# Performance work log

Measured on AMD Instinct MI355X. Metric: run time of the kernel, lower is better.

The kernel has to match this reference:

```python
import jax, jax.numpy as jnp
import numpy as np
from jax.scipy.linalg import expm

D_LOGIC = 128
D_MEM = 16
SO_DIM = D_MEM * (D_MEM - 1) // 2  # 120


def _linear_init(key, fan_in, shape):
    bound = 1.0 / np.sqrt(fan_in)
    return jax.random.uniform(key, shape, jnp.float32, -bound, bound)


def setup_inputs() -> dict:
    key = jax.random.key(0)
    ks = jax.random.split(key, 14)
    B, S = 4, 128
    return {
        "x_logic": jax.random.normal(ks[0], (B, S, D_LOGIC), jnp.float32),
        "x_memory": jax.random.normal(ks[1], (B, S, D_MEM), jnp.float32),
        # W_Q / W_K
        "Wq": _linear_init(ks[2], D_LOGIC, (D_LOGIC, D_LOGIC)),
        "bq": _linear_init(ks[3], D_LOGIC, (D_LOGIC,)),
        "Wk": _linear_init(ks[4], D_LOGIC, (D_LOGIC, D_LOGIC)),
        "bk": _linear_init(ks[5], D_LOGIC, (D_LOGIC,)),
        # gamma_net: Linear(d_logic, 2*d_logic) -> Tanh -> Linear(2*d_logic, so_dim)
        "W1": _linear_init(ks[6], D_LOGIC, (2 * D_LOGIC, D_LOGIC)),
        "b1": _linear_init(ks[7], D_LOGIC, (2 * D_LOGIC,)),
        "W2": _linear_init(ks[8], 2 * D_LOGIC, (SO_DIM, 2 * D_LOGIC)),
        "b2": _linear_init(ks[9], 2 * D_LOGIC, (SO_DIM,)),
        # out_proj: Linear(d_memory, d_memory)
        "Wo": _linear_init(ks[10], D_MEM, (D_MEM, D_MEM)),
        "bo": _linear_init(ks[11], D_MEM, (D_MEM,)),
    }


def reference(x_logic, x_memory, Wq, bq, Wk, bk, W1, b1, W2, b2, Wo, bo):
    B, S, d_logic = x_logic.shape
    dm = x_memory.shape[-1]

    # attention over logic stream
    Q = x_logic @ Wq.T + bq
    K = x_logic @ Wk.T + bk
    attn = jax.nn.softmax(
        jnp.einsum("bjd,bid->bji", Q, K) / jnp.sqrt(jnp.float32(d_logic)), axis=-1
    )  # [B, S(j), S(i)]

    # per-pair Lie-algebra params: delta[b,j,i] = x_logic[b,j] - x_logic[b,i]
    delta = x_logic[:, :, None, :] - x_logic[:, None, :, :]  # [B,S,S,d_logic]
    h = jnp.tanh(delta @ W1.T + b1)
    lie = h @ W2.T + b2  # [B,S,S,so_dim]

    # scatter into skew-symmetric matrices [B,S,S,dm,dm]
    r, c = np.triu_indices(dm, k=1)
    skew = jnp.zeros((B, S, S, dm, dm), x_logic.dtype)
    skew = skew.at[..., r, c].set(lie)
    skew = skew.at[..., c, r].set(-lie)

    # Lie-group exponential -> orthogonal transport matrices
    T_all = expm(skew)  # [B,S,S,dm,dm]

    # transported[b,j,i,:] = T[b,j,i] @ x_memory[b,i]
    transported = jnp.einsum("bjide,bie->bjid", T_all, x_memory)

    # attention-weighted aggregation over i
    settled = jnp.einsum("bji,bjid->bjd", attn, transported)  # [B,S,dm]

    out = settled @ Wo.T + bo
    return out, T_all
```

## Files before the change

### kernel.cpp

```cpp
#include <hip/hip_runtime.h>
#include <hip/hip_fp16.h>

#define S_LEN 128
#define DLOG  128
#define DMEM  16
#define SO    120
#define HDIM  256

typedef _Float16 v8h __attribute__((ext_vector_type(8)));
typedef __fp16 v2hf __attribute__((ext_vector_type(2)));
typedef float v4f __attribute__((ext_vector_type(4)));

union PkU { v2hf h; unsigned u; };
union V8U { v8h v; int u[4]; };

__device__ __forceinline__ v8h splat8(float x) {
  _Float16 h = (_Float16)x;
  v8h v = {h, h, h, h, h, h, h, h};
  return v;
}

__global__ __launch_bounds__(512) void qku_kernel(
    const float* __restrict__ xl, const float* __restrict__ Wq,
    const float* __restrict__ bq, const float* __restrict__ Wk,
    const float* __restrict__ bk, const float* __restrict__ W1,
    float* __restrict__ Q, float* __restrict__ K, float* __restrict__ u) {
  int bj = blockIdx.x, t = threadIdx.x;
  __shared__ float xs[128];
  if (t < 128) xs[t] = xl[bj * 128 + t];
  __syncthreads();
  const float* wr;
  float acc;
  int o;
  if (t < 128) {
    o = t; wr = Wq + o * 128; acc = bq[o];
  } else if (t < 256) {
    o = t - 128; wr = Wk + o * 128; acc = bk[o];
  } else {
    o = t - 256; wr = W1 + o * 128; acc = 0.f;
  }
  #pragma unroll 4
  for (int d = 0; d < 128; ++d) acc = fmaf(xs[d], wr[d], acc);
  if (t < 128) Q[bj * 128 + o] = acc;
  else if (t < 256) K[bj * 128 + o] = acc;
  else u[bj * 256 + o] = acc;
}

__global__ __launch_bounds__(128) void attn_kernel(
    const float* __restrict__ Q, const float* __restrict__ K,
    float* __restrict__ attn) {
  int bj = blockIdx.x, b = bj >> 7, i = threadIdx.x;
  __shared__ float qs[128];
  __shared__ float red[128];
  qs[i] = Q[bj * 128 + i];
  __syncthreads();
  const float* kr = K + (b * 128 + i) * 128;
  float s = 0.f;
  #pragma unroll 4
  for (int d = 0; d < 128; ++d) s = fmaf(qs[d], kr[d], s);
  s *= 0.08838834764831845f;
  red[i] = s;
  __syncthreads();
  for (int off = 64; off; off >>= 1) {
    if (i < off) red[i] = fmaxf(red[i], red[i + off]);
    __syncthreads();
  }
  float m = red[0];
  __syncthreads();
  float e = expf(s - m);
  red[i] = e;
  __syncthreads();
  for (int off = 64; off; off >>= 1) {
    if (i < off) red[i] += red[i + off];
    __syncthreads();
  }
  attn[(size_t)bj * 128 + i] = e / red[0];
}

__global__ __launch_bounds__(256) void w2prep_kernel(
    const float* __restrict__ W2g, _Float16* __restrict__ w2h) {
  int idx = (blockIdx.x * 256 + threadIdx.x) * 4;
  float4 v = *(const float4*)(W2g + idx);
  PkU u0, u1;
  u0.h = __builtin_amdgcn_cvt_pkrtz(v.x, v.y);
  u1.h = __builtin_amdgcn_cvt_pkrtz(v.z, v.w);
  uint2 pk = {u0.u, u1.u};
  *(uint2*)(w2h + idx) = pk;
}

__global__ __launch_bounds__(256) void h_from_u_kernel(
    const float* __restrict__ u, const float* __restrict__ b1,
    _Float16* __restrict__ hG) {
  int tid = blockIdx.x * 256 + threadIdx.x;
  #pragma unroll
  for (int g = 0; g < 4; ++g) {
    int unit = tid + g * 524288;
    int p = unit >> 5;
    int o0 = (unit & 31) * 8;
    int bj = p >> 7;
    int b = bj >> 7;
    int i = p & 127;
    const float* uj = u + bj * 256 + o0;
    const float* ui = u + (size_t)(b * 128 + i) * 256 + o0;
    const float* bb = b1 + o0;
    float4 j0 = *(const float4*)uj, j1 = *(const float4*)(uj + 4);
    float4 i0 = *(const float4*)ui, i1 = *(const float4*)(ui + 4);
    float4 c0 = *(const float4*)bb, c1 = *(const float4*)(bb + 4);
    float xv[8] = {j0.x - i0.x + c0.x, j0.y - i0.y + c0.y,
                   j0.z - i0.z + c0.z, j0.w - i0.w + c0.w,
                   j1.x - i1.x + c1.x, j1.y - i1.y + c1.y,
                   j1.z - i1.z + c1.z, j1.w - i1.w + c1.w};
    float rv[8];
    #pragma unroll
    for (int k = 0; k < 8; ++k) {
      float x = xv[k];
      float ax = fabsf(x);
      float e = __expf(-2.f * ax);
      float r = __fdividef(1.f - e, 1.f + e);
      rv[k] = copysignf(r, x);
    }
    V8U out;
    #pragma unroll
    for (int k = 0; k < 4; ++k) {
      PkU pu;
      pu.h = __builtin_amdgcn_cvt_pkrtz(rv[2 * k], rv[2 * k + 1]);
      out.u[k] = (int)pu.u;
    }
    *(v8h*)(hG + (size_t)p * 512 + o0) = out.v;
  }
}

__global__ __launch_bounds__(512) void lie_kernel(
    const _Float16* __restrict__ w2h, const float* __restrict__ b2g,
    float* __restrict__ Tg) {
  __shared__ _Float16 w2t[128 * 136];
  int t = threadIdx.x, lane = t & 63;
  int wu = __builtin_amdgcn_readfirstlane(t >> 6);
  int pbase = blockIdx.x * 128 + wu * 16;
  int nn = lane & 15, q = lane >> 4;
  const _Float16* hf = (const _Float16*)Tg;

  for (int idx = t; idx < 1088; idx += 512) w2t[16320 + idx] = (_Float16)0.f;

  v4f acc[8];
  #pragma unroll
  for (int tt = 0; tt < 8; ++tt) acc[tt] = (v4f){0.f, 0.f, 0.f, 0.f};

  const _Float16* hrow = hf + (size_t)(pbase + nn) * 512;
  for (int khalf = 0; khalf < 2; ++khalf) {
    __syncthreads();
    for (int idx = t; idx < 1920; idx += 512) {
      int row = idx >> 4, cu = (idx & 15) * 8;
      *(v8h*)(w2t + row * 136 + cu) =
          *(const v8h*)(w2h + row * 256 + khalf * 128 + cu);
    }
    __syncthreads();
    #pragma unroll
    for (int ks = 0; ks < 4; ++ks) {
      v8h ah = *(const v8h*)(hrow + khalf * 128 + ks * 32 + 8 * q);
      #pragma unroll
      for (int tt = 0; tt < 8; ++tt) {
        const v8h bf = *(const v8h*)(w2t + (16 * tt + nn) * 136 + ks * 32 + 8 * q);
        acc[tt] = __builtin_amdgcn_mfma_f32_16x16x32_f16(ah, bf, acc[tt], 0, 0, 0);
      }
    }
  }

  _Float16* hw = (_Float16*)Tg;
  #pragma unroll
  for (int tt = 0; tt < 8; ++tt) {
    int n16 = 16 * tt + nn;
    if (n16 < 120) {
      float bb = b2g[n16];
      #pragma unroll
      for (int reg = 0; reg < 4; ++reg) {
        size_t p = (size_t)(pbase + 4 * q + reg);
        hw[p * 512 + 256 + n16] = (_Float16)(acc[tt][reg] + bb);
      }
    }
  }
}

__device__ __forceinline__ void split8(const float* x, v8h& hi, v8h& lo) {
  union U { v8h v; v2hf p[4]; } H, L;
  #pragma unroll
  for (int i = 0; i < 4; ++i) {
    float a = x[2 * i], b = x[2 * i + 1];
    v2hf h = __builtin_amdgcn_cvt_pkrtz(a, b);
    float ra = (float)h[0], rb = (float)h[1];
    v2hf l = __builtin_amdgcn_cvt_pkrtz(a - ra, b - rb);
    H.p[i] = h;
    L.p[i] = l;
  }
  hi = H.v;
  lo = L.v;
}

__device__ __forceinline__ int lie_idx(int rr, int cc) {
  return 15 * rr - ((rr * (rr - 1)) >> 1) + cc - rr - 1;
}

__global__ __launch_bounds__(256) void expm_kernel(
    float* __restrict__ Tg, const float* __restrict__ attn,
    const float* __restrict__ xm, float* __restrict__ part) {
  __shared__ char lds[12288] __attribute__((aligned(16)));
  __shared__ float sred[4][16];
  int t = threadIdx.x, lane = t & 63;
  int wu = __builtin_amdgcn_readfirstlane(t >> 6);
  int pbase = blockIdx.x * 8 + wu * 2;
  int nn = lane & 15, q = lane >> 4, b8 = (q & 1) * 8;
  char* wb = lds + wu * 3072;
  _Float16* lieS = (_Float16*)wb;
  float* ErB = (float*)(wb + 512);
  const _Float16* hf = (const _Float16*)Tg;

  int idxA = ((2 * (q & 1)) * 16 + nn) * 4;
  int idxB = idxA + 64;

  float scv[2];
  int sv[2];
  #pragma unroll
  for (int j = 0; j < 2; ++j) {
    size_t p = (size_t)(pbase + j);
    _Float16 a0 = (lane < 120) ? hf[p * 512 + 256 + lane] : (_Float16)0.f;
    _Float16 a1 = (lane < 56) ? hf[p * 512 + 320 + lane] : (_Float16)0.f;
    lieS[j * 128 + lane] = a0;
    lieS[j * 128 + 64 + lane] = a1;
    float f0 = (float)a0, f1 = (float)a1;
    float s2 = f0 * f0 + f1 * f1;
    #pragma unroll
    for (int off = 1; off < 64; off <<= 1) s2 += __shfl_xor(s2, off, 64);
    float bound = sqrtf(s2);
    int s = 0;
    while (bound > 1.0f && s < 12) { bound *= 0.5f; s++; }
    sv[j] = __builtin_amdgcn_readfirstlane(s);
    scv[j] = ldexpf(1.0f, -s);
  }
  asm volatile("s_waitcnt lgkmcnt(0)" ::: "memory");

  V8U Apk[2], BfA[2];
  v4f Af[2];
  #pragma unroll
  for (int j = 0; j < 2; ++j) {
    const _Float16* lp = lieS + j * 128;
    float sc = scv[j];
    float av[8];
    #pragma unroll
    for (int jj = 0; jj < 8; ++jj) {
      int c = b8 + jj;
      int rr = min(nn, c), c2 = max(nn, c);
      float lv = (c == nn) ? 0.f : (float)lp[lie_idx(rr, c2)];
      av[jj] = (c == nn) ? 0.f : ((c > nn) ? lv : -lv) * sc;
    }
    #pragma unroll
    for (int i = 0; i < 4; ++i) {
      PkU u;
      u.h = __builtin_amdgcn_cvt_pkrtz(av[2 * i], av[2 * i + 1]);
      Apk[j].u[i] = (int)u.u;
      BfA[j].u[i] = Apk[j].u[i] ^ 0x80008000;
    }
    #pragma unroll
    for (int reg = 0; reg < 4; ++reg) {
      int r = 4 * q + reg;
      int rr = min(r, nn), c2 = max(r, nn);
      float lv = (r == nn) ? 0.f : (float)lp[lie_idx(rr, c2)];
      Af[j][reg] = (r == nn) ? 0.f : ((nn > r) ? lv : -lv) * sc;
    }
  }

  V8U IC1, IC2;
  #pragma unroll
  for (int i = 0; i < 4; ++i) {
    float d0 = (b8 + 2 * i == nn) ? 1.f : 0.f;
    float d1 = (b8 + 2 * i + 1 == nn) ? 1.f : 0.f;
    PkU u1, u2;
    u1.h = __builtin_amdgcn_cvt_pkrtz(10.666667f * d0, 10.666667f * d1);
    u2.h = __builtin_amdgcn_cvt_pkrtz(2.1333333f * d0, 2.1333333f * d1);
    IC1.u[i] = (int)u1.u;
    IC2.u[i] = (int)u2.u;
  }

  v4f z4 = {0.f, 0.f, 0.f, 0.f};

  v4f cB[2];
  #pragma unroll
  for (int j = 0; j < 2; ++j)
    cB[j] = __builtin_amdgcn_mfma_f32_16x16x32_f16(Apk[j].v, BfA[j].v, z4, 0, 0, 0);

  V8U fB[2];
  #pragma unroll
  for (int j = 0; j < 2; ++j) {
    PkU u0, u1;
    u0.h = __builtin_amdgcn_cvt_pkrtz(cB[j][0], cB[j][1]);
    u1.h = __builtin_amdgcn_cvt_pkrtz(cB[j][2], cB[j][3]);
    fB[j].u[0] = __builtin_amdgcn_ds_bpermute(idxA, (int)u0.u);
    fB[j].u[1] = __builtin_amdgcn_ds_bpermute(idxA, (int)u1.u);
    fB[j].u[2] = __builtin_amdgcn_ds_bpermute(idxB, (int)u0.u);
    fB[j].u[3] = __builtin_amdgcn_ds_bpermute(idxB, (int)u1.u);
  }

  v4f cB2[2];
  #pragma unroll
  for (int j = 0; j < 2; ++j)
    cB2[j] = __builtin_amdgcn_mfma_f32_16x16x32_f16(fB[j].v, fB[j].v, z4, 0, 0, 0);

  V8U fB2[2];
  #pragma unroll
  for (int j = 0; j < 2; ++j) {
    PkU u0, u1;
    u0.h = __builtin_amdgcn_cvt_pkrtz(cB2[j][0], cB2[j][1]);
    u1.h = __builtin_amdgcn_cvt_pkrtz(cB2[j][2], cB2[j][3]);
    fB2[j].u[0] = __builtin_amdgcn_ds_bpermute(idxA, (int)u0.u);
    fB2[j].u[1] = __builtin_amdgcn_ds_bpermute(idxA, (int)u1.u);
    fB2[j].u[2] = __builtin_amdgcn_ds_bpermute(idxB, (int)u0.u);
    fB2[j].u[3] = __builtin_amdgcn_ds_bpermute(idxB, (int)u1.u);
  }

  v8h k1a = splat8(7.9365079e-4f);
  v8h k1b = splat8(0.17777778f);
  v8h k2a = splat8(8.8183422e-5f);
  v8h k2b = splat8(2.5396825e-2f);
  V8U M1[2], M2[2];
  #pragma unroll
  for (int j = 0; j < 2; ++j) {
    M1[j].v = fB2[j].v * k1a + (fB[j].v * k1b + IC1.v);
    M2[j].v = fB2[j].v * k2a + (fB[j].v * k2b + IC2.v);
  }

  v4f Cc[2], Qc[2];
  #pragma unroll
  for (int j = 0; j < 2; ++j) {
    v4f c3m = __builtin_amdgcn_mfma_f32_16x16x32_f16(M1[j].v, fB2[j].v, z4, 0, 0, 0);
    v4f c4m = __builtin_amdgcn_mfma_f32_16x16x32_f16(M2[j].v, fB2[j].v, z4, 0, 0, 0);
    #pragma unroll
    for (int reg = 0; reg < 4; ++reg) {
      float dg = (4 * q + reg == nn) ? 1.f : 0.f;
      Cc[j][reg] = fmaf(c3m[reg], 2.44140625e-4f,
                        fmaf(cB[j][reg], 0.25f, dg + Af[j][reg]));
      Qc[j][reg] = fmaf(c4m[reg], 2.44140625e-4f, cB[j][reg] * 0.083333333f);
    }
  }

  V8U fQ[2];
  #pragma unroll
  for (int j = 0; j < 2; ++j) {
    PkU u0, u1;
    u0.h = __builtin_amdgcn_cvt_pkrtz(Qc[j][0], Qc[j][1]);
    u1.h = __builtin_amdgcn_cvt_pkrtz(Qc[j][2], Qc[j][3]);
    fQ[j].u[0] = __builtin_amdgcn_ds_bpermute(idxA, (int)u0.u);
    fQ[j].u[1] = __builtin_amdgcn_ds_bpermute(idxA, (int)u1.u);
    fQ[j].u[2] = __builtin_amdgcn_ds_bpermute(idxB, (int)u0.u);
    fQ[j].u[3] = __builtin_amdgcn_ds_bpermute(idxB, (int)u1.u);
  }

  v4f E[2];
  #pragma unroll
  for (int j = 0; j < 2; ++j) {
    v4f c5 = __builtin_amdgcn_mfma_f32_16x16x32_f16(Apk[j].v, fQ[j].v, z4, 0, 0, 0);
    E[j] = Cc[j] + c5 * 0.5f;
  }

  int smax = max(sv[0], sv[1]);
  for (int it = 0; it < smax; ++it) {
    #pragma unroll
    for (int j = 0; j < 2; ++j) {
      if (it < sv[j]) {
        float* Erp = ErB + j * 320;
        PkU u0, u1;
        u0.h = __builtin_amdgcn_cvt_pkrtz(E[j][0], E[j][1]);
        u1.h = __builtin_amdgcn_cvt_pkrtz(E[j][2], E[j][3]);
        V8U bfe;
        bfe.u[0] = __builtin_amdgcn_ds_bpermute(idxA, (int)u0.u);
        bfe.u[1] = __builtin_amdgcn_ds_bpermute(idxA, (int)u1.u);
        bfe.u[2] = __builtin_amdgcn_ds_bpermute(idxB, (int)u0.u);
        bfe.u[3] = __builtin_amdgcn_ds_bpermute(idxB, (int)u1.u);
        #pragma unroll
        for (int reg = 0; reg < 4; ++reg)
          Erp[(4 * q + reg) * 20 + nn] = E[j][reg];
        asm volatile("s_waitcnt lgkmcnt(0)" ::: "memory");
        float4 a0 = *(const float4*)(Erp + nn * 20 + b8);
        float4 a1 = *(const float4*)(Erp + nn * 20 + b8 + 4);
        float xa[8] = {a0.x, a0.y, a0.z, a0.w, a1.x, a1.y, a1.z, a1.w};
        v8h ahi, alo;
        split8(xa, ahi, alo);
        v8h Ecat = (q < 2) ? ahi : alo;
        v4f z = {0.f, 0.f, 0.f, 0.f};
        E[j] = __builtin_amdgcn_mfma_f32_16x16x32_f16(Ecat, bfe.v, z, 0, 0, 0);
      }
    }
  }

  float pacc[4] = {0.f, 0.f, 0.f, 0.f};
  #pragma unroll
  for (int j = 0; j < 2; ++j) {
    int p = pbase + j;
    float* dst = Tg + (size_t)p * 256;
    #pragma unroll
    for (int reg = 0; reg < 4; ++reg)
      dst[(4 * q + reg) * 16 + nn] = E[j][reg];
    int b = p >> 14, i = p & 127;
    float xv = xm[((b << 7) + i) * 16 + nn];
    float aw = attn[(size_t)p] * xv;
    #pragma unroll
    for (int reg = 0; reg < 4; ++reg)
      pacc[reg] = fmaf(aw, E[j][reg], pacc[reg]);
  }
  #pragma unroll
  for (int reg = 0; reg < 4; ++reg) {
    #pragma unroll
    for (int off = 1; off < 16; off <<= 1)
      pacc[reg] += __shfl_xor(pacc[reg], off, 64);
  }
  if (nn == 0) {
    #pragma unroll
    for (int reg = 0; reg < 4; ++reg) sred[wu][4 * q + reg] = pacc[reg];
  }
  __syncthreads();
  if (t < 16)
    part[(size_t)blockIdx.x * 16 + t] =
        sred[0][t] + sred[1][t] + sred[2][t] + sred[3][t];
}

__global__ __launch_bounds__(64) void settle_fin_kernel(
    const float* __restrict__ part, const float* __restrict__ Wo,
    const float* __restrict__ bo, float* __restrict__ outp) {
  int bj = blockIdx.x, t = threadIdx.x;
  int r = t & 15, e0 = t >> 4;
  const float* pb = part + (size_t)bj * 256;
  float s = pb[e0 * 16 + r] + pb[(e0 + 4) * 16 + r] +
            pb[(e0 + 8) * 16 + r] + pb[(e0 + 12) * 16 + r];
  __shared__ float sf[64];
  sf[t] = s;
  __syncthreads();
  if (t < 16) sf[t] = sf[t] + sf[16 + t] + sf[32 + t] + sf[48 + t];
  __syncthreads();
  if (t < 16) {
    float o = bo[t];
    const float* wr = Wo + t * 16;
    #pragma unroll
    for (int c = 0; c < 16; ++c) o = fmaf(wr[c], sf[c], o);
    outp[bj * 16 + t] = o;
  }
}

extern "C" void kernel_launch(void* const* d_in, const int* in_sizes, int n_in,
                              void* d_out, int out_size, void* d_ws,
                              size_t ws_size, hipStream_t stream) {
  const float* xl = (const float*)d_in[0];
  const float* xm = (const float*)d_in[1];
  const float* Wq = (const float*)d_in[2];
  const float* bq = (const float*)d_in[3];
  const float* Wk = (const float*)d_in[4];
  const float* bk = (const float*)d_in[5];
  const float* W1 = (const float*)d_in[6];
  const float* b1 = (const float*)d_in[7];
  const float* W2 = (const float*)d_in[8];
  const float* b2 = (const float*)d_in[9];
  const float* Wo = (const float*)d_in[10];
  const float* bo = (const float*)d_in[11];
  float* outp = (float*)d_out;
  float* Tg = outp + 8192;
  float* wsf = (float*)d_ws;
  float* Q = wsf;
  float* K = wsf + 65536;
  float* attn = wsf + 131072;
  _Float16* w2h = (_Float16*)Q;
  float* u = wsf + 196608;
  float* part = wsf + 196608;

  hipLaunchKernelGGL(qku_kernel, dim3(512), dim3(512), 0, stream, xl, Wq, bq, Wk, bk, W1, Q, K, u);
  hipLaunchKernelGGL(attn_kernel, dim3(512), dim3(128), 0, stream, Q, K, attn);
  hipLaunchKernelGGL(w2prep_kernel, dim3(30), dim3(256), 0, stream, W2, w2h);
  hipLaunchKernelGGL(h_from_u_kernel, dim3(2048), dim3(256), 0, stream, u, b1, (_Float16*)Tg);
  hipLaunchKernelGGL(lie_kernel, dim3(512), dim3(512), 0, stream, w2h, b2, Tg);
  hipLaunchKernelGGL(expm_kernel, dim3(8192), dim3(256), 0, stream, Tg, attn, xm, part);
  hipLaunchKernelGGL(settle_fin_kernel, dim3(512), dim3(64), 0, stream, part, Wo, bo, outp);
}
```

Measured before the change: 204.1 us.

## Write dense skew matrices from lie kernel and fold W2 prep into h kernel

The lie kernel now scatters each Lie parameter straight into a dense 16x16 fp16 skew-symmetric layout, with the negated transpose and a zeroed diagonal, in the scratch area of the output buffer. The expm kernel can then load its MFMA operand rows with one vector load instead of staging 120 values in LDS and gathering them through triangular index maths, which also shrinks its LDS use. The norm bound changes to half the Frobenius norm because each entry is now stored twice. Separately, the W2 fp16 conversion runs as extra blocks of the h_from_u kernel, removing one launch; the cost is scattered 2-byte writes in the lie kernel and a larger intermediate footprint per pair.

```diff
diff --git a/kernel.cpp b/kernel.cpp
--- a/kernel.cpp
+++ b/kernel.cpp
@@ -77,20 +77,20 @@
   attn[(size_t)bj * 128 + i] = e / red[0];
 }
 
-__global__ __launch_bounds__(256) void w2prep_kernel(
-    const float* __restrict__ W2g, _Float16* __restrict__ w2h) {
-  int idx = (blockIdx.x * 256 + threadIdx.x) * 4;
-  float4 v = *(const float4*)(W2g + idx);
-  PkU u0, u1;
-  u0.h = __builtin_amdgcn_cvt_pkrtz(v.x, v.y);
-  u1.h = __builtin_amdgcn_cvt_pkrtz(v.z, v.w);
-  uint2 pk = {u0.u, u1.u};
-  *(uint2*)(w2h + idx) = pk;
-}
-
 __global__ __launch_bounds__(256) void h_from_u_kernel(
     const float* __restrict__ u, const float* __restrict__ b1,
-    _Float16* __restrict__ hG) {
+    _Float16* __restrict__ hG, const float* __restrict__ W2g,
+    _Float16* __restrict__ w2h) {
+  if (blockIdx.x >= 2048) {
+    int idx = ((blockIdx.x - 2048) * 256 + threadIdx.x) * 4;
+    float4 v = *(const float4*)(W2g + idx);
+    PkU u0, u1;
+    u0.h = __builtin_amdgcn_cvt_pkrtz(v.x, v.y);
+    u1.h = __builtin_amdgcn_cvt_pkrtz(v.z, v.w);
+    uint2 pk = {u0.u, u1.u};
+    *(uint2*)(w2h + idx) = pk;
+    return;
+  }
   int tid = blockIdx.x * 256 + threadIdx.x;
   #pragma unroll
   for (int g = 0; g < 4; ++g) {
@@ -172,12 +172,24 @@
     int n16 = 16 * tt + nn;
     if (n16 < 120) {
       float bb = b2g[n16];
+      float fr_ = floorf((31.0f - sqrtf(961.0f - 8.0f * (float)n16)) * 0.5f);
+      int r = (int)fr_;
+      int Sr = 15 * r - ((r * (r - 1)) >> 1);
+      int c = n16 - Sr + r + 1;
       #pragma unroll
       for (int reg = 0; reg < 4; ++reg) {
         size_t p = (size_t)(pbase + 4 * q + reg);
-        hw[p * 512 + 256 + n16] = (_Float16)(acc[tt][reg] + bb);
+        _Float16 hv = (_Float16)(acc[tt][reg] + bb);
+        _Float16* Ab = hw + p * 512 + 256;
+        Ab[r * 16 + c] = hv;
+        Ab[c * 16 + r] = -hv;
       }
     }
+  }
+  #pragma unroll
+  for (int reg = 0; reg < 4; ++reg) {
+    size_t p = (size_t)(pbase + 4 * q + reg);
+    (hw + p * 512 + 256)[nn * 17] = (_Float16)0.f;
   }
 }
 
@@ -196,22 +208,16 @@
   lo = L.v;
 }
 
-__device__ __forceinline__ int lie_idx(int rr, int cc) {
-  return 15 * rr - ((rr * (rr - 1)) >> 1) + cc - rr - 1;
-}
-
 __global__ __launch_bounds__(256) void expm_kernel(
     float* __restrict__ Tg, const float* __restrict__ attn,
     const float* __restrict__ xm, float* __restrict__ part) {
-  __shared__ char lds[12288] __attribute__((aligned(16)));
+  __shared__ char lds[10240] __attribute__((aligned(16)));
   __shared__ float sred[4][16];
   int t = threadIdx.x, lane = t & 63;
   int wu = __builtin_amdgcn_readfirstlane(t >> 6);
   int pbase = blockIdx.x * 8 + wu * 2;
   int nn = lane & 15, q = lane >> 4, b8 = (q & 1) * 8;
-  char* wb = lds + wu * 3072;
-  _Float16* lieS = (_Float16*)wb;
-  float* ErB = (float*)(wb + 512);
+  float* ErB = (float*)(lds + wu * 2560);
   const _Float16* hf = (const _Float16*)Tg;
 
   int idxA = ((2 * (q & 1)) * 16 + nn) * 4;
@@ -219,53 +225,37 @@
 
   float scv[2];
   int sv[2];
+  V8U Apk[2], BfA[2];
+  v4f Af[2];
   #pragma unroll
   for (int j = 0; j < 2; ++j) {
     size_t p = (size_t)(pbase + j);
-    _Float16 a0 = (lane < 120) ? hf[p * 512 + 256 + lane] : (_Float16)0.f;
-    _Float16 a1 = (lane < 56) ? hf[p * 512 + 320 + lane] : (_Float16)0.f;
-    lieS[j * 128 + lane] = a0;
-    lieS[j * 128 + 64 + lane] = a1;
-    float f0 = (float)a0, f1 = (float)a1;
-    float s2 = f0 * f0 + f1 * f1;
+    const _Float16* Ap = hf + p * 512 + 256;
+    v8h rowh = *(const v8h*)(Ap + nn * 16 + b8);
+    float s2 = 0.f;
+    #pragma unroll
+    for (int k = 0; k < 8; ++k) {
+      float xf = (float)rowh[k];
+      s2 = fmaf(xf, xf, s2);
+    }
     #pragma unroll
     for (int off = 1; off < 64; off <<= 1) s2 += __shfl_xor(s2, off, 64);
-    float bound = sqrtf(s2);
+    float bound = 0.5f * sqrtf(s2);
     int s = 0;
     while (bound > 1.0f && s < 12) { bound *= 0.5f; s++; }
     sv[j] = __builtin_amdgcn_readfirstlane(s);
     scv[j] = ldexpf(1.0f, -s);
-  }
-  asm volatile("s_waitcnt lgkmcnt(0)" ::: "memory");
-
-  V8U Apk[2], BfA[2];
-  v4f Af[2];
-  #pragma unroll
-  for (int j = 0; j < 2; ++j) {
-    const _Float16* lp = lieS + j * 128;
-    float sc = scv[j];
-    float av[8];
-    #pragma unroll
-    for (int jj = 0; jj < 8; ++jj) {
-      int c = b8 + jj;
-      int rr = min(nn, c), c2 = max(nn, c);
-      float lv = (c == nn) ? 0.f : (float)lp[lie_idx(rr, c2)];
-      av[jj] = (c == nn) ? 0.f : ((c > nn) ? lv : -lv) * sc;
-    }
+    v8h sch = splat8(scv[j]);
+    V8U ap;
+    ap.v = rowh * sch;
     #pragma unroll
     for (int i = 0; i < 4; ++i) {
-      PkU u;
-      u.h = __builtin_amdgcn_cvt_pkrtz(av[2 * i], av[2 * i + 1]);
-      Apk[j].u[i] = (int)u.u;
-      BfA[j].u[i] = Apk[j].u[i] ^ 0x80008000;
-    }
-    #pragma unroll
-    for (int reg = 0; reg < 4; ++reg) {
-      int r = 4 * q + reg;
-      int rr = min(r, nn), c2 = max(r, nn);
-      float lv = (r == nn) ? 0.f : (float)lp[lie_idx(rr, c2)];
-      Af[j][reg] = (r == nn) ? 0.f : ((nn > r) ? lv : -lv) * sc;
-    }
+      Apk[j].u[i] = ap.u[i];
+      BfA[j].u[i] = ap.u[i] ^ 0x80008000;
+    }
+    #pragma unroll
+    for (int reg = 0; reg < 4; ++reg)
+      Af[j][reg] = (float)Ap[(4 * q + reg) * 16 + nn] * scv[j];
   }
 
   V8U IC1, IC2;
@@ -470,8 +460,7 @@
 
   hipLaunchKernelGGL(qku_kernel, dim3(512), dim3(512), 0, stream, xl, Wq, bq, Wk, bk, W1, Q, K, u);
   hipLaunchKernelGGL(attn_kernel, dim3(512), dim3(128), 0, stream, Q, K, attn);
-  hipLaunchKernelGGL(w2prep_kernel, dim3(30), dim3(256), 0, stream, W2, w2h);
-  hipLaunchKernelGGL(h_from_u_kernel, dim3(2048), dim3(256), 0, stream, u, b1, (_Float16*)Tg);
+  hipLaunchKernelGGL(h_from_u_kernel, dim3(2078), dim3(256), 0, stream, u, b1, (_Float16*)Tg, W2, w2h);
   hipLaunchKernelGGL(lie_kernel, dim3(512), dim3(512), 0, stream, w2h, b2, Tg);
   hipLaunchKernelGGL(expm_kernel, dim3(8192), dim3(256), 0, stream, Tg, attn, xm, part);
   hipLaunchKernelGGL(settle_fin_kernel, dim3(512), dim3(64), 0, stream, part, Wo, bo, outp);
```

Result: slower. 214.9 us (+5.3%).
